# Performance work log

Hardware: AMD Instinct MI355X
Metric: run time of the kernel (lower is better)

The kernel has to match this reference:

```python
import jax, jax.numpy as jnp
import numpy as np

B, C, H, W = 4, 512, 64, 64
C8 = C // 8


def setup_inputs() -> dict:
    key = jax.random.key(0)
    ks = jax.random.split(key, 12)
    s = lambda fan_in: 1.0 / np.sqrt(fan_in)
    return {
        "final_encoded": jax.random.normal(ks[0], (B, C, H, W), jnp.float32),
        "total": jax.random.normal(ks[1], (B, C, H, W), jnp.float32),
        # 1x1 conv weights (out, in) and biases
        "Wq": jax.random.normal(ks[2], (C8, C), jnp.float32) * s(C),
        "bq": jax.random.normal(ks[3], (C8,), jnp.float32) * s(C),
        "Wk": jax.random.normal(ks[4], (C8, C), jnp.float32) * s(C),
        "bk": jax.random.normal(ks[5], (C8,), jnp.float32) * s(C),
        "Wv": jax.random.normal(ks[6], (C, C), jnp.float32) * s(C),
        "bv": jax.random.normal(ks[7], (C,), jnp.float32) * s(C),
        # learned additive positional tensors
        "height_tensor": jax.random.normal(ks[8], (1, C8, H, 1), jnp.float32),
        "width_tensor": jax.random.normal(ks[9], (1, C8, 1, W), jnp.float32),
        "gamma": jnp.zeros((1,), jnp.float32),
    }


def reference(final_encoded, total, Wq, bq, Wk, bk, Wv, bv, height_tensor, width_tensor, gamma):
    b, c, h, w = final_encoded.shape
    c8 = c // 8
    hw = h * w
    # 1x1 convs as channel matmuls
    q = jnp.einsum("oc,bchw->bohw", Wq, total) + bq[None, :, None, None]
    k = jnp.einsum("oc,bchw->bohw", Wk, final_encoded) + bk[None, :, None, None]
    v = jnp.einsum("oc,bchw->bohw", Wv, final_encoded) + bv[None, :, None, None]
    pq = q.reshape(b, c8, hw).transpose(0, 2, 1)   # [B, HW, C8]
    pk = k.reshape(b, c8, hw)                      # [B, C8, HW]
    pv = v.reshape(b, c, hw)                       # [B, C, HW]
    energy = jnp.einsum("bnc,bcm->bnm", pq, pk)    # [B, HW, HW] content energy
    pos = (height_tensor + width_tensor).reshape(c8, hw)  # [C8, HW] additive positional bias basis
    energy = energy + jnp.einsum("bnc,cm->bnm", pq, pos)
    attention = jax.nn.softmax(energy, axis=-1)
    # out = bmm(value, attention^T)
    out = jnp.einsum("bcm,bnm->bcn", pv, attention).reshape(b, c, h, w)
    return gamma * out + final_encoded
```

## Files before the change

kernel.cpp:

```cpp
#include <hip/hip_runtime.h>
#include <hip/hip_bf16.h>
#include <type_traits>

#define B_   4
#define C_   512
#define C8_  64
#define HW_  4096

typedef short bf16x8 __attribute__((ext_vector_type(8)));
typedef float f32x4  __attribute__((ext_vector_type(4)));

__device__ __forceinline__ unsigned short f2bf(float f) {
  union { unsigned int i; float f; } x; x.f = f;
  unsigned int r = x.i + 0x7fffu + ((x.i >> 16) & 1u);
  return (unsigned short)(r >> 16);
}

__device__ __forceinline__ unsigned int cvtpk(float lo, float hi) {
  unsigned int r;
  asm("v_cvt_pk_bf16_f32 %0, %1, %2" : "=v"(r) : "v"(lo), "v"(hi));
  return r;
}

#define MFMA(a, b, c) __builtin_amdgcn_mfma_f32_16x16x32_bf16((a), (b), (c), 0, 0, 0)


__global__ __launch_bounds__(256) void proj_kernel(
    const float* __restrict__ total, const float* __restrict__ fe,
    const float* __restrict__ Wq, const float* __restrict__ bq,
    const float* __restrict__ Wk, const float* __restrict__ bk,
    const float* __restrict__ Wv, const float* __restrict__ bv,
    const float* __restrict__ ht, const float* __restrict__ wt,
    unsigned short* __restrict__ Qh, unsigned short* __restrict__ Kh,
    unsigned short* __restrict__ Vn) {
  __shared__ __align__(16) unsigned short Xs[64 * 72];
  __shared__ __align__(16) unsigned short Ws[128 * 72];
  const int t = threadIdx.x;
  const int b = blockIdx.z;
  const int y = blockIdx.y;
  const int x = blockIdx.x;
  const int m0 = x * 64;
  const int lane = t & 63, w = t >> 6, ln = lane & 15, quad = lane >> 4;

  if (y < 2) {
    const float* X = (y == 0) ? total : fe;
    const float* W = (y == 0) ? Wq : Wk;
    const float* bias = (y == 0) ? bq : bk;
    unsigned short* dst = (y == 0) ? Qh : Kh;

    f32x4 acc[4];
#pragma unroll
    for (int i = 0; i < 4; ++i) acc[i] = f32x4{0.f, 0.f, 0.f, 0.f};

    for (int kb = 0; kb < 8; ++kb) {
      const int c0 = kb * 64;
#pragma unroll
      for (int i = 0; i < 4; ++i) {
        int idx = t + i * 256; int o = idx >> 4, c4 = idx & 15;
        float4 wv = *(const float4*)&W[(size_t)o * C_ + c0 + c4 * 4];
        unsigned int p0 = f2bf(wv.x) | ((unsigned int)f2bf(wv.y) << 16);
        unsigned int p1 = f2bf(wv.z) | ((unsigned int)f2bf(wv.w) << 16);
        *(uint2*)&Ws[o * 72 + c4 * 4] = make_uint2(p0, p1);
      }
#pragma unroll
      for (int i = 0; i < 4; ++i) {
        int idx = t + i * 256; int rc = idx >> 4, mq = idx & 15;
        float4 xv = *(const float4*)&X[((size_t)b * C_ + c0 + rc) * HW_ + m0 + mq * 4];
        Xs[(mq * 4 + 0) * 72 + rc] = f2bf(xv.x);
        Xs[(mq * 4 + 1) * 72 + rc] = f2bf(xv.y);
        Xs[(mq * 4 + 2) * 72 + rc] = f2bf(xv.z);
        Xs[(mq * 4 + 3) * 72 + rc] = f2bf(xv.w);
      }
      __syncthreads();
      bf16x8 a0 = *(const bf16x8*)&Xs[(w * 16 + ln) * 72 + quad * 8];
      bf16x8 a1 = *(const bf16x8*)&Xs[(w * 16 + ln) * 72 + 32 + quad * 8];
#pragma unroll
      for (int nt = 0; nt < 4; ++nt) {
        bf16x8 b0 = *(const bf16x8*)&Ws[(nt * 16 + ln) * 72 + quad * 8];
        bf16x8 b1 = *(const bf16x8*)&Ws[(nt * 16 + ln) * 72 + 32 + quad * 8];
        acc[nt] = MFMA(a0, b0, acc[nt]);
        acc[nt] = MFMA(a1, b1, acc[nt]);
      }
      __syncthreads();
    }

    const int h = x;
#pragma unroll
    for (int nt = 0; nt < 4; ++nt) {
      const int o = nt * 16 + ln;
      const float bz = bias[o];
      const float hv = (y == 1) ? ht[o * 64 + h] : 0.0f;
#pragma unroll
      for (int r = 0; r < 4; ++r) {
        const int mloc = w * 16 + quad * 4 + r;
        float val = acc[nt][r] + bz + hv;
        if (y == 1) val += wt[o * 64 + mloc];
        const size_t idx = ((size_t)b * 512 + (size_t)(x * 4 + w) * 2 + (nt >> 1)) * 512
                         + ((nt & 1) * 2 + (ln >> 3)) * 128 + (quad * 4 + r) * 8 + (ln & 7);
        dst[idx] = f2bf(val);
      }
    }
  } else {
    const int o0 = (y - 2) * 128;
    f32x4 acc[2][4];
#pragma unroll
    for (int p = 0; p < 2; ++p)
#pragma unroll
      for (int i = 0; i < 4; ++i) acc[p][i] = f32x4{0.f, 0.f, 0.f, 0.f};

    for (int kb = 0; kb < 8; ++kb) {
      const int c0 = kb * 64;
#pragma unroll
      for (int i = 0; i < 8; ++i) {
        int idx = t + i * 256; int o = idx >> 4, c4 = idx & 15;
        float4 wv = *(const float4*)&Wv[(size_t)(o0 + o) * C_ + c0 + c4 * 4];
        unsigned int p0 = f2bf(wv.x) | ((unsigned int)f2bf(wv.y) << 16);
        unsigned int p1 = f2bf(wv.z) | ((unsigned int)f2bf(wv.w) << 16);
        *(uint2*)&Ws[o * 72 + c4 * 4] = make_uint2(p0, p1);
      }
#pragma unroll
      for (int i = 0; i < 4; ++i) {
        int idx = t + i * 256; int rc = idx >> 4, mq = idx & 15;
        float4 xv = *(const float4*)&fe[((size_t)b * C_ + c0 + rc) * HW_ + m0 + mq * 4];
        Xs[(mq * 4 + 0) * 72 + rc] = f2bf(xv.x);
        Xs[(mq * 4 + 1) * 72 + rc] = f2bf(xv.y);
        Xs[(mq * 4 + 2) * 72 + rc] = f2bf(xv.z);
        Xs[(mq * 4 + 3) * 72 + rc] = f2bf(xv.w);
      }
      __syncthreads();
      bf16x8 aW[2][2];
#pragma unroll
      for (int p = 0; p < 2; ++p) {
        aW[p][0] = *(const bf16x8*)&Ws[((w + 4 * p) * 16 + ln) * 72 + quad * 8];
        aW[p][1] = *(const bf16x8*)&Ws[((w + 4 * p) * 16 + ln) * 72 + 32 + quad * 8];
      }
#pragma unroll
      for (int nt = 0; nt < 4; ++nt) {
        bf16x8 b0 = *(const bf16x8*)&Xs[(nt * 16 + ln) * 72 + quad * 8];
        bf16x8 b1 = *(const bf16x8*)&Xs[(nt * 16 + ln) * 72 + 32 + quad * 8];
#pragma unroll
        for (int p = 0; p < 2; ++p) {
          acc[p][nt] = MFMA(aW[p][0], b0, acc[p][nt]);
          acc[p][nt] = MFMA(aW[p][1], b1, acc[p][nt]);
        }
      }
      __syncthreads();
    }

#pragma unroll
    for (int p = 0; p < 2; ++p) {
#pragma unroll
      for (int r = 0; r < 4; ++r) {
        const int cht = (o0 >> 4) + w + 4 * p;
        const float bz = bv[cht * 16 + quad * 4 + r];
#pragma unroll
        for (int nt = 0; nt < 4; ++nt) {
          const size_t idx = (((size_t)b * 32 + cht) * 128 + (size_t)x * 2 + (nt >> 1)) * 512
                           + ((nt & 1) * 2 + (ln >> 3)) * 128 + (quad * 4 + r) * 8 + (ln & 7);
          Vn[idx] = f2bf(acc[p][nt][r] + bz);
        }
      }
    }
  }
}

__global__ __launch_bounds__(512, 4) void flash_kernel(
    const unsigned short* __restrict__ Qh, const unsigned short* __restrict__ Kh,
    const unsigned short* __restrict__ Vn, const float* __restrict__ fe,
    const float* __restrict__ gamma, float* __restrict__ out) {
  __shared__ __align__(16) unsigned short Ps[2][64 * 64];
  __shared__ float Red[2][64];

  const int t = threadIdx.x;
  const int n = blockIdx.x;
  const int xcd = n & 7;
  const int b = xcd & 3;
  const int ch0 = (xcd >> 2) * 256;
  const int q0 = (n >> 3) * 64;
  const int lane = t & 63, w = t >> 6, ln = lane & 15, quad = lane >> 4;
  const int qt = w & 3;
  const int kh = w >> 2;
  const int swz = (ln & 7) << 4;

  const unsigned short* Qb = Qh + (size_t)b * 512 * 512;
  const unsigned short* Kb = Kh + (size_t)b * 512 * 512;
  const unsigned short* Vbase = Vn + ((size_t)b * 32 + (ch0 >> 4)) * (128 * 512);

  const bf16x8 aq0 = *(const bf16x8*)&Qb[((size_t)((q0 >> 4) + qt) * 2 + 0) * 512 + lane * 8];
  const bf16x8 aq1 = *(const bf16x8*)&Qb[((size_t)((q0 >> 4) + qt) * 2 + 1) * 512 + lane * 8];

  float Sacc = 0.f;
  f32x4 acc[2][4];
#pragma unroll
  for (int mt = 0; mt < 2; ++mt)
#pragma unroll
    for (int nt = 0; nt < 4; ++nt) acc[mt][nt] = f32x4{0.f, 0.f, 0.f, 0.f};

  bf16x8 kf[2][2];
  bf16x8 vf[2][2];

  auto loadK = [&](int it) {
#pragma unroll
    for (int nt = 0; nt < 2; ++nt)
#pragma unroll
      for (int hf = 0; hf < 2; ++hf)
        kf[nt][hf] = *(const bf16x8*)&Kb[((size_t)(it * 4 + kh * 2 + nt) * 2 + hf) * 512 + lane * 8];
  };
  auto loadV = [&](int it) {
#pragma unroll
    for (int mt = 0; mt < 2; ++mt)
#pragma unroll
      for (int kc = 0; kc < 2; ++kc)
        vf[mt][kc] = *(const bf16x8*)&Vbase[(((size_t)(w * 2 + mt)) * 128 + it * 2 + kc) * 512 + lane * 8];
  };

  loadK(0);
  loadV(0);

  const int qrow = qt * 16 + ln;

  for (int it = 0; it < 64; ++it) {
    char* Pcur = (char*)Ps[it & 1];
    __builtin_amdgcn_s_setprio(1);
    f32x4 e0 = MFMA(kf[0][0], aq0, (f32x4{0.f, 0.f, 0.f, 0.f}));
    e0 = MFMA(kf[0][1], aq1, e0);
    f32x4 e1 = MFMA(kf[1][0], aq0, (f32x4{0.f, 0.f, 0.f, 0.f}));
    e1 = MFMA(kf[1][1], aq1, e1);
    __builtin_amdgcn_s_setprio(0);
    if (it < 63) loadK(it + 1);
    {
      const float p0 = __expf(e0[0] - 20.0f), p1 = __expf(e0[1] - 20.0f);
      const float p2 = __expf(e0[2] - 20.0f), p3 = __expf(e0[3] - 20.0f);
      Sacc += (p0 + p1) + (p2 + p3);
      *(uint2*)(Pcur + ((qrow * 128 + kh * 64 + 0 * 32 + quad * 8) ^ swz)) =
          make_uint2(cvtpk(p0, p1), cvtpk(p2, p3));
      const float s0 = __expf(e1[0] - 20.0f), s1 = __expf(e1[1] - 20.0f);
      const float s2 = __expf(e1[2] - 20.0f), s3 = __expf(e1[3] - 20.0f);
      Sacc += (s0 + s1) + (s2 + s3);
      *(uint2*)(Pcur + ((qrow * 128 + kh * 64 + 1 * 32 + quad * 8) ^ swz)) =
          make_uint2(cvtpk(s0, s1), cvtpk(s2, s3));
    }
    asm volatile("s_waitcnt lgkmcnt(0)" ::: "memory");
    __builtin_amdgcn_s_barrier();
    asm volatile("" ::: "memory");
#pragma unroll
    for (int kc = 0; kc < 2; ++kc) {
      bf16x8 bp[4];
#pragma unroll
      for (int nt = 0; nt < 4; ++nt)
        bp[nt] = *(const bf16x8*)(Pcur + ((((nt * 16 + ln) * 128 + kc * 64 + quad * 16)) ^ swz));
      __builtin_amdgcn_s_setprio(1);
#pragma unroll
      for (int mt = 0; mt < 2; ++mt)
#pragma unroll
        for (int nt = 0; nt < 4; ++nt)
          acc[mt][nt] = MFMA(vf[mt][kc], bp[nt], acc[mt][nt]);
      __builtin_amdgcn_s_setprio(0);
    }
    if (it < 63) loadV(it + 1);
  }

  {
    float s = Sacc;
    s += __shfl_xor(s, 16);
    s += __shfl_xor(s, 32);
    if (quad == 0) Red[kh][qrow] = s;
  }
  __syncthreads();
  float rsv[4];
#pragma unroll
  for (int nt = 0; nt < 4; ++nt)
    rsv[nt] = 1.0f / (Red[0][nt * 16 + ln] + Red[1][nt * 16 + ln]);

  const float g = gamma[0];
#pragma unroll
  for (int mt = 0; mt < 2; ++mt) {
#pragma unroll
    for (int r = 0; r < 4; ++r) {
      const int ch = ch0 + w * 32 + mt * 16 + quad * 4 + r;
      const size_t base = ((size_t)b * C_ + ch) * HW_ + q0;
#pragma unroll
      for (int nt = 0; nt < 4; ++nt) {
        const size_t idx = base + nt * 16 + ln;
        out[idx] = g * (acc[mt][nt][r] * rsv[nt]) + fe[idx];
      }
    }
  }
}

extern "C" void kernel_launch(void* const* d_in, const int* in_sizes, int n_in,
                              void* d_out, int out_size, void* d_ws, size_t ws_size,
                              hipStream_t stream) {
  const float* fe    = (const float*)d_in[0];
  const float* total = (const float*)d_in[1];
  const float* Wq    = (const float*)d_in[2];
  const float* bq    = (const float*)d_in[3];
  const float* Wk    = (const float*)d_in[4];
  const float* bk    = (const float*)d_in[5];
  const float* Wv    = (const float*)d_in[6];
  const float* bv    = (const float*)d_in[7];
  const float* ht    = (const float*)d_in[8];
  const float* wt    = (const float*)d_in[9];
  const float* gamma = (const float*)d_in[10];
  float* out = (float*)d_out;

  unsigned short* Qh = (unsigned short*)d_ws;
  unsigned short* Kh = Qh + (size_t)B_ * HW_ * C8_;
  unsigned short* Vn = Kh + (size_t)B_ * HW_ * C8_;

  proj_kernel<<<dim3(64, 6, B_), 256, 0, stream>>>(total, fe, Wq, bq, Wk, bk,
                                                   Wv, bv, ht, wt, Qh, Kh, Vn);
  flash_kernel<<<dim3(512), 512, 0, stream>>>(Qh, Kh, Vn, fe, gamma, out);
}
```

Baseline: 262.9 us.

## Software-pipeline QK energy one step ahead of PV, fold scaling into exp2

The attention loop is restructured so each iteration computes the QK energies and exponentials for the next key block into the other P buffer while doing PV MFMAs on the current one, with a single barrier per iteration. The log2(e) factor is folded into Q during projection and the constant shift into the MFMA accumulator init, so the exponential becomes a raw v_exp_f32. The projection kernel also loads four channel rows per thread and converts with packed bf16 conversions, writing uint2 to LDS instead of scalar shorts. The goal is to overlap exp work with matrix math and cut VALU and LDS store cost, at the price of more registers and more complex barrier logic.

```diff
diff --git a/kernel.cpp b/kernel.cpp
--- a/kernel.cpp
+++ b/kernel.cpp
@@ -1,6 +1,5 @@
 #include <hip/hip_runtime.h>
 #include <hip/hip_bf16.h>
-#include <type_traits>
 
 #define B_   4
 #define C_   512
@@ -22,7 +21,16 @@
   return r;
 }
 
+__device__ __forceinline__ float fexp2(float x) {
+  float r;
+  asm("v_exp_f32 %0, %1" : "=v"(r) : "v"(x));
+  return r;
+}
+
 #define MFMA(a, b, c) __builtin_amdgcn_mfma_f32_16x16x32_bf16((a), (b), (c), 0, 0, 0)
+
+#define LOG2E 1.44269504f
+#define NEG20LOG2E -28.8539008f
 
 
 __global__ __launch_bounds__(256) void proj_kernel(
@@ -41,6 +49,7 @@
   const int x = blockIdx.x;
   const int m0 = x * 64;
   const int lane = t & 63, w = t >> 6, ln = lane & 15, quad = lane >> 4;
+  const int rc4 = t >> 4, mq = t & 15;
 
   if (y < 2) {
     const float* X = (y == 0) ? total : fe;
@@ -57,19 +66,18 @@
 #pragma unroll
       for (int i = 0; i < 4; ++i) {
         int idx = t + i * 256; int o = idx >> 4, c4 = idx & 15;
-        float4 wv = *(const float4*)&W[(size_t)o * C_ + c0 + c4 * 4];
-        unsigned int p0 = f2bf(wv.x) | ((unsigned int)f2bf(wv.y) << 16);
-        unsigned int p1 = f2bf(wv.z) | ((unsigned int)f2bf(wv.w) << 16);
-        *(uint2*)&Ws[o * 72 + c4 * 4] = make_uint2(p0, p1);
-      }
-#pragma unroll
-      for (int i = 0; i < 4; ++i) {
-        int idx = t + i * 256; int rc = idx >> 4, mq = idx & 15;
-        float4 xv = *(const float4*)&X[((size_t)b * C_ + c0 + rc) * HW_ + m0 + mq * 4];
-        Xs[(mq * 4 + 0) * 72 + rc] = f2bf(xv.x);
-        Xs[(mq * 4 + 1) * 72 + rc] = f2bf(xv.y);
-        Xs[(mq * 4 + 2) * 72 + rc] = f2bf(xv.z);
-        Xs[(mq * 4 + 3) * 72 + rc] = f2bf(xv.w);
+        f32x4 wv = *(const f32x4*)&W[(size_t)o * C_ + c0 + c4 * 4];
+        *(uint2*)&Ws[o * 72 + c4 * 4] = make_uint2(cvtpk(wv[0], wv[1]), cvtpk(wv[2], wv[3]));
+      }
+      {
+        f32x4 xv[4];
+#pragma unroll
+        for (int k = 0; k < 4; ++k)
+          xv[k] = *(const f32x4*)&X[((size_t)b * C_ + c0 + rc4 * 4 + k) * HW_ + m0 + mq * 4];
+#pragma unroll
+        for (int j = 0; j < 4; ++j)
+          *(uint2*)&Xs[(mq * 4 + j) * 72 + rc4 * 4] =
+              make_uint2(cvtpk(xv[0][j], xv[1][j]), cvtpk(xv[2][j], xv[3][j]));
       }
       __syncthreads();
       bf16x8 a0 = *(const bf16x8*)&Xs[(w * 16 + ln) * 72 + quad * 8];
@@ -95,6 +103,7 @@
         const int mloc = w * 16 + quad * 4 + r;
         float val = acc[nt][r] + bz + hv;
         if (y == 1) val += wt[o * 64 + mloc];
+        if (y == 0) val *= LOG2E;
         const size_t idx = ((size_t)b * 512 + (size_t)(x * 4 + w) * 2 + (nt >> 1)) * 512
                          + ((nt & 1) * 2 + (ln >> 3)) * 128 + (quad * 4 + r) * 8 + (ln & 7);
         dst[idx] = f2bf(val);
@@ -113,19 +122,18 @@
 #pragma unroll
       for (int i = 0; i < 8; ++i) {
         int idx = t + i * 256; int o = idx >> 4, c4 = idx & 15;
-        float4 wv = *(const float4*)&Wv[(size_t)(o0 + o) * C_ + c0 + c4 * 4];
-        unsigned int p0 = f2bf(wv.x) | ((unsigned int)f2bf(wv.y) << 16);
-        unsigned int p1 = f2bf(wv.z) | ((unsigned int)f2bf(wv.w) << 16);
-        *(uint2*)&Ws[o * 72 + c4 * 4] = make_uint2(p0, p1);
-      }
-#pragma unroll
-      for (int i = 0; i < 4; ++i) {
-        int idx = t + i * 256; int rc = idx >> 4, mq = idx & 15;
-        float4 xv = *(const float4*)&fe[((size_t)b * C_ + c0 + rc) * HW_ + m0 + mq * 4];
-        Xs[(mq * 4 + 0) * 72 + rc] = f2bf(xv.x);
-        Xs[(mq * 4 + 1) * 72 + rc] = f2bf(xv.y);
-        Xs[(mq * 4 + 2) * 72 + rc] = f2bf(xv.z);
-        Xs[(mq * 4 + 3) * 72 + rc] = f2bf(xv.w);
+        f32x4 wv = *(const f32x4*)&Wv[(size_t)(o0 + o) * C_ + c0 + c4 * 4];
+        *(uint2*)&Ws[o * 72 + c4 * 4] = make_uint2(cvtpk(wv[0], wv[1]), cvtpk(wv[2], wv[3]));
+      }
+      {
+        f32x4 xv[4];
+#pragma unroll
+        for (int k = 0; k < 4; ++k)
+          xv[k] = *(const f32x4*)&fe[((size_t)b * C_ + c0 + rc4 * 4 + k) * HW_ + m0 + mq * 4];
+#pragma unroll
+        for (int j = 0; j < 4; ++j)
+          *(uint2*)&Xs[(mq * 4 + j) * 72 + rc4 * 4] =
+              make_uint2(cvtpk(xv[0][j], xv[1][j]), cvtpk(xv[2][j], xv[3][j]));
       }
       __syncthreads();
       bf16x8 aW[2][2];
@@ -189,6 +197,8 @@
   const bf16x8 aq0 = *(const bf16x8*)&Qb[((size_t)((q0 >> 4) + qt) * 2 + 0) * 512 + lane * 8];
   const bf16x8 aq1 = *(const bf16x8*)&Qb[((size_t)((q0 >> 4) + qt) * 2 + 1) * 512 + lane * 8];
 
+  const f32x4 CINIT = {NEG20LOG2E, NEG20LOG2E, NEG20LOG2E, NEG20LOG2E};
+
   float Sacc = 0.f;
   f32x4 acc[2][4];
 #pragma unroll
@@ -214,50 +224,77 @@
         vf[mt][kc] = *(const bf16x8*)&Vbase[(((size_t)(w * 2 + mt)) * 128 + it * 2 + kc) * 512 + lane * 8];
   };
 
+  const int qrow = qt * 16 + ln;
+
+  auto writeP = [&](f32x4 e0, f32x4 e1, char* Pw) {
+    const float p0 = fexp2(e0[0]), p1 = fexp2(e0[1]);
+    const float p2 = fexp2(e0[2]), p3 = fexp2(e0[3]);
+    Sacc += (p0 + p1) + (p2 + p3);
+    *(uint2*)(Pw + ((qrow * 128 + kh * 64 + quad * 8) ^ swz)) =
+        make_uint2(cvtpk(p0, p1), cvtpk(p2, p3));
+    const float s0 = fexp2(e1[0]), s1 = fexp2(e1[1]);
+    const float s2 = fexp2(e1[2]), s3 = fexp2(e1[3]);
+    Sacc += (s0 + s1) + (s2 + s3);
+    *(uint2*)(Pw + ((qrow * 128 + kh * 64 + 32 + quad * 8) ^ swz)) =
+        make_uint2(cvtpk(s0, s1), cvtpk(s2, s3));
+  };
+
   loadK(0);
   loadV(0);
 
-  const int qrow = qt * 16 + ln;
+  {
+    f32x4 e0 = MFMA(kf[0][0], aq0, CINIT);
+    e0 = MFMA(kf[0][1], aq1, e0);
+    f32x4 e1 = MFMA(kf[1][0], aq0, CINIT);
+    e1 = MFMA(kf[1][1], aq1, e1);
+    writeP(e0, e1, (char*)Ps[0]);
+  }
+  loadK(1);
+  asm volatile("s_waitcnt lgkmcnt(0)" ::: "memory");
+  __builtin_amdgcn_s_barrier();
+  asm volatile("" ::: "memory");
 
   for (int it = 0; it < 64; ++it) {
-    char* Pcur = (char*)Ps[it & 1];
+    char* Prd = (char*)Ps[it & 1];
+    char* Pwr = (char*)Ps[(it + 1) & 1];
+    bf16x8 bp0[4];
+#pragma unroll
+    for (int nt = 0; nt < 4; ++nt)
+      bp0[nt] = *(const bf16x8*)(Prd + ((((nt * 16 + ln) * 128 + quad * 16)) ^ swz));
+    if (it < 63) {
+      __builtin_amdgcn_s_setprio(1);
+      f32x4 e0 = MFMA(kf[0][0], aq0, CINIT);
+      e0 = MFMA(kf[0][1], aq1, e0);
+      f32x4 e1 = MFMA(kf[1][0], aq0, CINIT);
+      e1 = MFMA(kf[1][1], aq1, e1);
+      __builtin_amdgcn_s_setprio(0);
+      if (it < 62) loadK(it + 2);
+      writeP(e0, e1, Pwr);
+    }
     __builtin_amdgcn_s_setprio(1);
-    f32x4 e0 = MFMA(kf[0][0], aq0, (f32x4{0.f, 0.f, 0.f, 0.f}));
-    e0 = MFMA(kf[0][1], aq1, e0);
-    f32x4 e1 = MFMA(kf[1][0], aq0, (f32x4{0.f, 0.f, 0.f, 0.f}));
-    e1 = MFMA(kf[1][1], aq1, e1);
+#pragma unroll
+    for (int mt = 0; mt < 2; ++mt)
+#pragma unroll
+      for (int nt = 0; nt < 4; ++nt)
+        acc[mt][nt] = MFMA(vf[mt][0], bp0[nt], acc[mt][nt]);
     __builtin_amdgcn_s_setprio(0);
-    if (it < 63) loadK(it + 1);
-    {
-      const float p0 = __expf(e0[0] - 20.0f), p1 = __expf(e0[1] - 20.0f);
-      const float p2 = __expf(e0[2] - 20.0f), p3 = __expf(e0[3] - 20.0f);
-      Sacc += (p0 + p1) + (p2 + p3);
-      *(uint2*)(Pcur + ((qrow * 128 + kh * 64 + 0 * 32 + quad * 8) ^ swz)) =
-          make_uint2(cvtpk(p0, p1), cvtpk(p2, p3));
-      const float s0 = __expf(e1[0] - 20.0f), s1 = __expf(e1[1] - 20.0f);
-      const float s2 = __expf(e1[2] - 20.0f), s3 = __expf(e1[3] - 20.0f);
-      Sacc += (s0 + s1) + (s2 + s3);
-      *(uint2*)(Pcur + ((qrow * 128 + kh * 64 + 1 * 32 + quad * 8) ^ swz)) =
-          make_uint2(cvtpk(s0, s1), cvtpk(s2, s3));
-    }
-    asm volatile("s_waitcnt lgkmcnt(0)" ::: "memory");
-    __builtin_amdgcn_s_barrier();
-    asm volatile("" ::: "memory");
-#pragma unroll
-    for (int kc = 0; kc < 2; ++kc) {
-      bf16x8 bp[4];
+    bf16x8 bp1[4];
+#pragma unroll
+    for (int nt = 0; nt < 4; ++nt)
+      bp1[nt] = *(const bf16x8*)(Prd + ((((nt * 16 + ln) * 128 + 64 + quad * 16)) ^ swz));
+    __builtin_amdgcn_s_setprio(1);
+#pragma unroll
+    for (int mt = 0; mt < 2; ++mt)
 #pragma unroll
       for (int nt = 0; nt < 4; ++nt)
-        bp[nt] = *(const bf16x8*)(Pcur + ((((nt * 16 + ln) * 128 + kc * 64 + quad * 16)) ^ swz));
-      __builtin_amdgcn_s_setprio(1);
-#pragma unroll
-      for (int mt = 0; mt < 2; ++mt)
-#pragma unroll
-        for (int nt = 0; nt < 4; ++nt)
-          acc[mt][nt] = MFMA(vf[mt][kc], bp[nt], acc[mt][nt]);
-      __builtin_amdgcn_s_setprio(0);
-    }
-    if (it < 63) loadV(it + 1);
+        acc[mt][nt] = MFMA(vf[mt][1], bp1[nt], acc[mt][nt]);
+    __builtin_amdgcn_s_setprio(0);
+    if (it < 63) {
+      loadV(it + 1);
+      asm volatile("s_waitcnt lgkmcnt(0)" ::: "memory");
+      __builtin_amdgcn_s_barrier();
+      asm volatile("" ::: "memory");
+    }
   }
 
   {
```

Result: faster. 228.2 us (-13.2%).
